# Optimization experiments

Measured on AMD Instinct MI355X. Metric: run time of the kernel, lower is better.

The kernel has to match this reference:

```python
import jax, jax.numpy as jnp
import numpy as np

N, E, U, L = 10000, 320000, 256, 3


def setup_inputs() -> dict:
    key = jax.random.key(0)
    ks = jax.random.split(key, 16)
    s = 0.05
    p = {}
    p["pos"] = jax.random.normal(ks[0], (N, 2), jnp.float32)
    p["edge_attr_in"] = jax.random.uniform(ks[1], (E, 1), jnp.float32)
    p["edge_index"] = jax.random.randint(ks[2], (2, E), 0, N)
    p["Wp"] = jax.random.normal(ks[3], (2, U), jnp.float32) * s
    p["bp"] = jnp.zeros((U,), jnp.float32)
    p["Wa"] = jax.random.normal(ks[4], (1, U), jnp.float32) * s
    p["ba"] = jnp.zeros((U,), jnp.float32)
    p["W1"] = jax.random.normal(ks[5], (L, U, U), jnp.float32) * s
    p["b1"] = jnp.zeros((L, U), jnp.float32)
    p["W2"] = jax.random.normal(ks[6], (L, U, U), jnp.float32) * s
    p["b2"] = jnp.zeros((L, U), jnp.float32)
    p["We"] = jax.random.normal(ks[7], (L + 1, U, U), jnp.float32) * s
    p["be"] = jnp.zeros((L + 1, U), jnp.float32)
    p["Ws"] = jax.random.normal(ks[8], (L + 1, U, U), jnp.float32) * s
    p["Wt"] = jax.random.normal(ks[9], (L + 1, U, U), jnp.float32) * s
    p["Wm1"] = jax.random.normal(ks[10], (U + 1, U // 2), jnp.float32) * s
    p["bm1"] = jnp.zeros((U // 2,), jnp.float32)
    p["alpha"] = 0.25 * jnp.ones((1,), jnp.float32)  # PReLU default slope
    p["Wm2"] = jax.random.normal(ks[11], (U // 2, 1), jnp.float32) * s
    p["bm2"] = jnp.zeros((1,), jnp.float32)
    return p


def _forward(pos, edge_attr_in, edge_index, Wp, bp, Wa, ba, W1, b1, W2, b2,
             We, be, Ws, Wt, Wm1, bm1, alpha, Wm2, bm2):
    src, dst = edge_index[0], edge_index[1]
    x = pos @ Wp + bp                      # [N, U]
    e = edge_attr_in @ Wa + ba             # [E, U]

    def edge_update(x, e, l):
        # ResEdgeLinear: residual edge update from endpoint nodes + edge feats
        return e + jax.nn.relu(e @ We[l] + x[src] @ Ws[l] + x[dst] @ Wt[l] + be[l])

    for l in range(L):
        # ResNodeConv: gated gather-linear-scatter with residual
        gate = jax.nn.sigmoid(e)                                   # [E, U]
        msg = gate * (x[src] @ W2[l] + b2[l])                      # [E, U]
        agg = jax.ops.segment_sum(msg, dst, num_segments=N)        # [N, U]
        x_new = x + jax.nn.relu(x @ W1[l] + b1[l] + agg)
        e_new = edge_update(x, e, l)  # simultaneous update: both use old (x, e)
        x, e = x_new, e_new
    e = edge_update(x, e, L)

    h = jnp.concatenate([e, edge_attr_in[:, :1]], axis=-1) @ Wm1 + bm1
    h = jnp.where(h > 0, h, alpha * h)  # PReLU
    return h @ Wm2 + bm2                # [E, 1] logits


def reference(pos, edge_attr_in, edge_index, Wp, bp, Wa, ba, W1, b1, W2, b2,
              We, be, Ws, Wt, Wm1, bm1, alpha, Wm2, bm2):
    return _forward(pos, edge_attr_in, edge_index, Wp, bp, Wa, ba, W1, b1,
                    W2, b2, We, be, Ws, Wt, Wm1, bm1, alpha, Wm2, bm2)
```

## Files before the change

### kernel.cpp

```cpp
#include <hip/hip_runtime.h>
#include <hip/hip_bf16.h>
#include <stdint.h>

#define N_NODES 10000
#define N_EDGES 320000

using bf16x8 = __attribute__((ext_vector_type(8))) short;
using fp32x4 = __attribute__((ext_vector_type(4))) float;
using u16x8 = __attribute__((ext_vector_type(8))) unsigned short;
using i32x4 = __attribute__((ext_vector_type(4))) int;

__device__ __forceinline__ float bf2f(unsigned short u) {
  union { unsigned int i; float f; } v; v.i = ((unsigned int)u) << 16; return v.f;
}
__device__ __forceinline__ unsigned short f2bf(float f) {
  union { float f; unsigned int i; } v; v.f = f;
  unsigned int x = v.i;
  x += 0x7fffu + ((x >> 16) & 1u);
  return (unsigned short)(x >> 16);
}
__device__ __forceinline__ unsigned int f2bf_pk(float lo, float hi) {
  __hip_bfloat162 h = __float22bfloat162_rn(float2{lo, hi});
  union { __hip_bfloat162 h; unsigned int u; } cv; cv.h = h; return cv.u;
}

#define A_POS 0
#define A_EA 20000
#define A_WP 340000
#define A_BP 340512
#define A_WA 340768
#define A_BA 341024
#define A_W1 341280
#define A_B1 537888
#define A_W2 538656
#define A_B2 735264
#define A_WE 736032
#define A_BE 998176
#define A_WS 999200
#define A_WT 1261344
#define A_WM1 1523488
#define A_BM1 1556384
#define A_AL 1556512
#define A_WM2 1556544
#define A_BM2 1556672
#define ARENA_USED 1556673
#define ARENA_TOT 1556736

__constant__ int g_off[19] = {A_POS, A_EA, A_WP, A_BP, A_WA, A_BA, A_W1, A_B1,
                              A_W2, A_B2, A_WE, A_BE, A_WS, A_WT, A_WM1,
                              A_BM1, A_AL, A_WM2, A_BM2};

struct Ptrs { const void* p[19]; };

__global__ void k_detect(const unsigned short* wpraw, int* flag, int* deg) {
  int i = blockIdx.x * 256 + threadIdx.x;
  if (i < N_NODES) deg[i] = 0;
  if (blockIdx.x == 0) {
    __shared__ int cnt;
    int tid = threadIdx.x;
    if (tid == 0) cnt = 0;
    __syncthreads();
    float v0 = bf2f(wpraw[tid]);
    float v1 = bf2f(wpraw[256 + tid]);
    int big = (fabsf(v0) > 100.f ? 1 : 0) + (fabsf(v1) > 100.f ? 1 : 0);
    atomicAdd(&cnt, big);
    __syncthreads();
    if (tid == 0) *flag = (cnt > 10) ? 1 : 0;
  }
}

__global__ void k_cast(Ptrs ptrs, const int* __restrict__ flag,
                       unsigned short* __restrict__ arena) {
  int a = blockIdx.x * 256 + threadIdx.x;
  if (a >= ARENA_USED) return;
  int z = 0;
#pragma unroll
  for (int j = 1; j < 19; ++j) if (a >= g_off[j]) z = j;
  int i = a - g_off[z];
  float v;
  if (*flag) v = ((const float*)ptrs.p[z])[i];
  else       v = bf2f(((const unsigned short*)ptrs.p[z])[i]);
  arena[a] = f2bf(v);
}

__global__ void k_prep(const unsigned short* __restrict__ arena,
                       unsigned short* nodeBT, unsigned short* WeT,
                       unsigned short* Wm1T, unsigned short* biascat) {
  int z = blockIdx.z;
  int i = blockIdx.x * 256 + threadIdx.x;
  if (z == 19) {
    if (i < 3072) {
      int l = i >> 10, j = i & 1023;
      unsigned short v = 0;
      if (j < 256) v = arena[A_B1 + l * 256 + j];
      else if (j < 512) v = arena[A_B2 + l * 256 + (j - 256)];
      biascat[i] = v;
    } else if (i < 3584) {
      biascat[i] = 0;
    }
    return;
  }
  const unsigned short* src; unsigned short* dst; int srcN = 256;
  if (z < 3)       {                 src = arena + A_W1 + z * 65536; dst = nodeBT + z * 262144; }
  else if (z < 6)  { int l = z - 3;  src = arena + A_W2 + l * 65536; dst = nodeBT + l * 262144 + 65536; }
  else if (z < 10) { int l = z - 6;  src = arena + A_WS + l * 65536;
                     dst = (l < 3) ? nodeBT + l * 262144 + 131072 : nodeBT + 786432; }
  else if (z < 14) { int l = z - 10; src = arena + A_WT + l * 65536;
                     dst = (l < 3) ? nodeBT + l * 262144 + 196608 : nodeBT + 786432 + 65536; }
  else if (z < 18) { int l = z - 14; src = arena + A_WE + l * 65536; dst = WeT + l * 65536; }
  else             { src = arena + A_WM1; dst = Wm1T; srcN = 128; }
  if (i < srcN * 256) {
    int k = i & 255, n = i >> 8;
    dst[i] = src[k * srcN + n];
  }
}

__global__ void k_pack(const unsigned short* __restrict__ src,
                       unsigned short* __restrict__ dst, int MT, int nchunks) {
  int c = blockIdx.x * 256 + threadIdx.x;
  if (c >= nchunks) return;
  int perg = MT * 512;
  int g = c / perg, r = c % perg;
  int ks = r / (64 * MT);
  int rem = r % (64 * MT);
  int mt = rem >> 6, lane = rem & 63;
  int q = lane >> 4, ll = lane & 15;
  int oc = g * (MT * 16) + (ll >> 2) * (MT * 4) + (ll & 3) + mt * 4;
  i32x4 v = *(const i32x4*)((const char*)src + ((long)oc << 9) + (ks << 6) + (q << 4));
  ((i32x4*)dst)[c] = v;
}

__global__ void k_init_x(const unsigned short* __restrict__ arena,
                         float* __restrict__ xf, unsigned short* __restrict__ xbf,
                         float* __restrict__ agg) {
  int n = blockIdx.x, c = threadIdx.x;
  float p0 = bf2f(arena[A_POS + 2 * n]), p1 = bf2f(arena[A_POS + 2 * n + 1]);
  float v = fmaf(p0, bf2f(arena[A_WP + c]),
                 fmaf(p1, bf2f(arena[A_WP + 256 + c]), bf2f(arena[A_BP + c])));
  long idx = ((long)n << 8) + c;
  xf[idx] = v;
  xbf[idx] = f2bf(v);
  agg[idx] = 0.f;
}

__global__ void k_hist(const int* __restrict__ dstA, int* __restrict__ deg) {
  int i = blockIdx.x * 256 + threadIdx.x;
  if (i < N_EDGES) {
    int d = dstA[i];
    if ((unsigned)d < N_NODES) atomicAdd(&deg[d], 1);
  }
}

__global__ void k_scan(const int* __restrict__ deg, int* __restrict__ rowptr,
                       int* __restrict__ cursor) {
  __shared__ int part[256];
  int tid = threadIdx.x;
  int base = tid * 40;
  int s = 0;
  for (int i = 0; i < 40; ++i) {
    int idx = base + i;
    if (idx < N_NODES) s += deg[idx];
  }
  part[tid] = s;
  __syncthreads();
  if (tid == 0) {
    int run = 0;
    for (int i = 0; i < 256; ++i) { int t = part[i]; part[i] = run; run += t; }
    rowptr[N_NODES] = run;
  }
  __syncthreads();
  int run = part[tid];
  for (int i = 0; i < 40; ++i) {
    int idx = base + i;
    if (idx < N_NODES) { rowptr[idx] = run; cursor[idx] = run; run += deg[idx]; }
  }
}

__global__ void k_fill(const int* __restrict__ dstA, const int* __restrict__ srcA,
                       const unsigned short* __restrict__ arena,
                       int* __restrict__ cursor, int* __restrict__ eid,
                       int* __restrict__ csrc, int* __restrict__ cdst,
                       unsigned short* __restrict__ eaC) {
  int i = blockIdx.x * 256 + threadIdx.x;
  if (i < N_EDGES) {
    int d = dstA[i]; if ((unsigned)d >= N_NODES) d = 0;
    int p = atomicAdd(&cursor[d], 1);
    if ((unsigned)p < N_EDGES) {
      eid[p] = i;
      int s = srcA[i]; if ((unsigned)s >= N_NODES) s = 0;
      csrc[p] = s;
      cdst[p] = d;
      eaC[p] = arena[A_EA + i];
    }
  }
}

#define SM_PITCH 528
#define XS_PITCH 144
#define EROWS 80
#define ECHUNKS 5
#define EDGE_BLOCKS (N_EDGES / EROWS)

template <bool NT, int ROWS, int BLK>
__device__ __forceinline__ void stage_tile(char* smc, const unsigned short* src,
                                           long rowBase) {
  int tid = threadIdx.x;
#pragma unroll
  for (int it = 0; it < ROWS * 32 / BLK; ++it) {
    int lin = it * BLK + tid;
    int row = lin >> 5, g = lin & 31;
    const i32x4* p = (const i32x4*)((const char*)src + ((rowBase + row) << 9) + (g << 4));
    i32x4 v = NT ? __builtin_nontemporal_load(p) : *p;
    *(i32x4*)(smc + row * SM_PITCH + (g << 4)) = v;
  }
}

template <int MT, int NTT>
__device__ __forceinline__ void gemm_swap(const char* smc, const unsigned short* WTp,
                                          int colBase, fp32x4 (&acc)[MT][NTT]) {
  const int lane = threadIdx.x & 63;
  const int q = lane >> 4, ll = lane & 15;
  const char* wbase = (const char*)WTp + ((long)colBase << 9) + (lane << 4);
  __builtin_amdgcn_s_setprio(1);
#pragma unroll
  for (int ks = 0; ks < 8; ++ks) {
    bf16x8 a[MT];
#pragma unroll
    for (int mt = 0; mt < MT; ++mt)
      a[mt] = *(const bf16x8*)(wbase + ((long)(ks * MT + mt) << 10));
    bf16x8 b[NTT];
#pragma unroll
    for (int nt = 0; nt < NTT; ++nt)
      b[nt] = *(const bf16x8*)(smc + (nt * 16 + ll) * SM_PITCH + (ks << 6) + (q << 4));
#pragma unroll
    for (int mt = 0; mt < MT; ++mt)
#pragma unroll
      for (int nt = 0; nt < NTT; ++nt)
        acc[mt][nt] = __builtin_amdgcn_mfma_f32_16x16x32_bf16(a[mt], b[nt], acc[mt][nt], 0, 0, 0);
  }
  __builtin_amdgcn_s_setprio(0);
}

template <int NTT>
__device__ __forceinline__ void edge_epilogue_cx(
    char* smc, char* xsw, const fp32x4 (&acc)[4][NTT], const int* s_src,
    const int* s_dst, const unsigned short* XW, int xw_pitch, int xs_off,
    int xt_off, const unsigned short* bePtr, int colBase, int lane) {
  const int q = lane >> 4, ll = lane & 15;
  const int cb = colBase + q * 16;
  u16x8 be0 = *(const u16x8*)(bePtr + cb);
  u16x8 be1 = *(const u16x8*)(bePtr + cb + 8);
  const int prow = lane >> 3;
  const int ppc = lane & 7;
  const int pcol = xs_off + colBase + ppc * 8;
  u16x8 pfA = *(const u16x8*)(XW + (long)s_src[prow] * xw_pitch + pcol);
  u16x8 pfB = *(const u16x8*)(XW + (long)s_src[8 + prow] * xw_pitch + pcol);
#pragma unroll
  for (int nt = 0; nt < NTT; ++nt) {
    *(u16x8*)(xsw + prow * XS_PITCH + ppc * 16) = pfA;
    *(u16x8*)(xsw + (8 + prow) * XS_PITCH + ppc * 16) = pfB;
    if (nt + 1 < NTT) {
      int elA = (nt + 1) * 16 + prow;
      pfA = *(const u16x8*)(XW + (long)s_src[elA] * xw_pitch + pcol);
      pfB = *(const u16x8*)(XW + (long)s_src[elA + 8] * xw_pitch + pcol);
    }
    int el = nt * 16 + ll;
    int dn = s_dst[el];
    const unsigned short* xtrow = XW + (long)dn * xw_pitch + xt_off + cb;
    u16x8 xt0 = *(const u16x8*)(xtrow);
    u16x8 xt1 = *(const u16x8*)(xtrow + 8);
    u16x8 xs0 = *(const u16x8*)(xsw + ll * XS_PITCH + q * 32);
    u16x8 xs1 = *(const u16x8*)(xsw + ll * XS_PITCH + q * 32 + 16);
    u16x8* slot = (u16x8*)(smc + el * SM_PITCH + cb * 2);
    u16x8 er0 = slot[0], er1 = slot[1];
    float f[16];
#pragma unroll
    for (int mt = 0; mt < 4; ++mt)
#pragma unroll
      for (int r = 0; r < 4; ++r) {
        int i = mt * 4 + r;
        float xsv = bf2f(i < 8 ? xs0[i] : xs1[i - 8]);
        float xtv = bf2f(i < 8 ? xt0[i] : xt1[i - 8]);
        float erv = bf2f(i < 8 ? er0[i] : er1[i - 8]);
        float bev = bf2f(i < 8 ? be0[i] : be1[i - 8]);
        float v = acc[mt][nt][r] + xsv + xtv + bev;
        v = fmaxf(v, 0.f);
        f[i] = erv + v;
      }
    union { u16x8 v; unsigned int w[4]; } O0, O1;
#pragma unroll
    for (int p = 0; p < 4; ++p) {
      O0.w[p] = f2bf_pk(f[2 * p], f[2 * p + 1]);
      O1.w[p] = f2bf_pk(f[8 + 2 * p], f[9 + 2 * p]);
    }
    slot[0] = O0.v;
    slot[1] = O1.v;
  }
}

__global__ __launch_bounds__(256, 3) void k_edge01(
    unsigned short* __restrict__ e, const unsigned short* __restrict__ WeT0,
    const unsigned short* __restrict__ WeT1,
    const unsigned short* __restrict__ XWa, const unsigned short* __restrict__ XWb,
    const unsigned short* __restrict__ arena, const unsigned short* __restrict__ eaC,
    const int* __restrict__ csrc, const int* __restrict__ cdst,
    float* __restrict__ agg) {
  __shared__ int4 sm4[EROWS * 33];
  __shared__ int4 xsb4[4 * 2304 / 16];
  __shared__ int s_src[EROWS];
  __shared__ int s_dst[EROWS];
  char* smc = (char*)sm4;
  const long tileBase = (long)blockIdx.x * EROWS;
  const int tid = threadIdx.x;
  const int wave = tid >> 6, lane = tid & 63;
  const int colBase = wave * 64;
  char* xsw = (char*)xsb4 + wave * 2304;

#pragma unroll
  for (int it = 0; it < EROWS * 32 / 256; ++it) {
    int lin = it * 256 + tid;
    int row = lin >> 5, g = lin & 31;
    float eav = bf2f(eaC[tileBase + row]);
    int c0 = g * 8;
    float f[8];
#pragma unroll
    for (int j = 0; j < 8; ++j)
      f[j] = fmaf(eav, bf2f(arena[A_WA + c0 + j]), bf2f(arena[A_BA + c0 + j]));
    union { bf16x8 v; unsigned int w[4]; } O;
#pragma unroll
    for (int p = 0; p < 4; ++p) O.w[p] = f2bf_pk(f[2 * p], f[2 * p + 1]);
    *(bf16x8*)(smc + row * SM_PITCH + (g << 4)) = O.v;
  }
  if (tid < EROWS) {
    long edge = tileBase + tid;
    int s = csrc[edge]; if ((unsigned)s >= N_NODES) s = 0;
    int d = cdst[edge]; if ((unsigned)d >= N_NODES) d = 0;
    s_src[tid] = s;
    s_dst[tid] = d;
  }
  __syncthreads();

  fp32x4 acc[4][ECHUNKS];
#pragma unroll
  for (int mt = 0; mt < 4; ++mt)
#pragma unroll
    for (int nt = 0; nt < ECHUNKS; ++nt) acc[mt][nt] = 0.f;
  gemm_swap<4, ECHUNKS>(smc, WeT0, colBase, acc);
  __syncthreads();
  edge_epilogue_cx<ECHUNKS>(smc, xsw, acc, s_src, s_dst, XWa, 1024, 512, 768,
                            arena + A_BE, colBase, lane);
  __syncthreads();

  {
    const int c = tid;
    float a = 0.f;
    int run = s_dst[0];
    for (int b8 = 0; b8 < EROWS; b8 += 8) {
      float evv[8], x2v[8];
#pragma unroll
      for (int j = 0; j < 8; ++j) {
        int row = b8 + j;
        evv[j] = bf2f(*(const unsigned short*)(smc + row * SM_PITCH + c * 2));
        x2v[j] = bf2f(XWb[(long)s_src[row] * 1024 + 256 + c]);
      }
#pragma unroll
      for (int j = 0; j < 8; ++j) {
        int d = s_dst[b8 + j];
        if (d != run) {
          atomicAdd(&agg[((long)run << 8) + c], a);
          a = 0.f;
          run = d;
        }
        float gate = 1.f / (1.f + __expf(-evv[j]));
        a = fmaf(gate, x2v[j], a);
      }
    }
    atomicAdd(&agg[((long)run << 8) + c], a);
  }

#pragma unroll
  for (int mt = 0; mt < 4; ++mt)
#pragma unroll
    for (int nt = 0; nt < ECHUNKS; ++nt) acc[mt][nt] = 0.f;
  gemm_swap<4, ECHUNKS>(smc, WeT1, colBase, acc);
  __syncthreads();
  edge_epilogue_cx<ECHUNKS>(smc, xsw, acc, s_src, s_dst, XWb, 1024, 512, 768,
                            arena + A_BE + 256, colBase, lane);
  __syncthreads();

#pragma unroll
  for (int it = 0; it < EROWS * 32 / 256; ++it) {
    int lin = it * 256 + tid;
    int row = lin >> 5, g = lin & 31;
    i32x4 v = *(const i32x4*)(smc + row * SM_PITCH + (g << 4));
    __builtin_nontemporal_store(v, (i32x4*)((char*)e + ((tileBase + row) << 9) + (g << 4)));
  }
}

__global__ __launch_bounds__(256, 3) void k_edge_last2(
    const unsigned short* __restrict__ e, const unsigned short* __restrict__ WeT2,
    const unsigned short* __restrict__ WeT3,
    const unsigned short* __restrict__ XW2, const unsigned short* __restrict__ XW3,
    const unsigned short* __restrict__ arena, const unsigned short* __restrict__ eaC,
    const int* __restrict__ csrc, const int* __restrict__ cdst,
    const unsigned short* __restrict__ Wm1T, const int* __restrict__ eid,
    const int* __restrict__ flag, void* __restrict__ out) {
  __shared__ int4 sm4[EROWS * 33];
  __shared__ int4 xsb4[4 * 2304 / 16];
  __shared__ int s_src[EROWS];
  __shared__ int s_dst[EROWS];
  __shared__ float part[EROWS * 4];
  char* smc = (char*)sm4;
  const long tileBase = (long)blockIdx.x * EROWS;
  const int tid = threadIdx.x;
  const int wave = tid >> 6, lane = tid & 63;
  const int q = lane >> 4, ll = lane & 15;
  const int colBase = wave * 64;
  char* xsw = (char*)xsb4 + wave * 2304;

  stage_tile<true, EROWS, 256>(smc, e, tileBase);
  if (tid < EROWS) {
    long edge = tileBase + tid;
    int s = csrc[edge]; if ((unsigned)s >= N_NODES) s = 0;
    int d = cdst[edge]; if ((unsigned)d >= N_NODES) d = 0;
    s_src[tid] = s;
    s_dst[tid] = d;
  }
  __syncthreads();

  fp32x4 acc[4][ECHUNKS];
#pragma unroll
  for (int mt = 0; mt < 4; ++mt)
#pragma unroll
    for (int nt = 0; nt < ECHUNKS; ++nt) acc[mt][nt] = 0.f;
  gemm_swap<4, ECHUNKS>(smc, WeT2, colBase, acc);
  __syncthreads();
  edge_epilogue_cx<ECHUNKS>(smc, xsw, acc, s_src, s_dst, XW2, 1024, 512, 768,
                            arena + A_BE + 2 * 256, colBase, lane);
  __syncthreads();

#pragma unroll
  for (int mt = 0; mt < 4; ++mt)
#pragma unroll
    for (int nt = 0; nt < ECHUNKS; ++nt) acc[mt][nt] = 0.f;
  gemm_swap<4, ECHUNKS>(smc, WeT3, colBase, acc);
  __syncthreads();
  edge_epilogue_cx<ECHUNKS>(smc, xsw, acc, s_src, s_dst, XW3, 512, 0, 256,
                            arena + A_BE + 3 * 256, colBase, lane);
  __syncthreads();

  fp32x4 acc2[2][ECHUNKS];
#pragma unroll
  for (int mt = 0; mt < 2; ++mt)
#pragma unroll
    for (int nt = 0; nt < ECHUNKS; ++nt) acc2[mt][nt] = 0.f;
  const int colBase2 = wave * 32;
  gemm_swap<2, ECHUNKS>(smc, Wm1T, colBase2, acc2);

  const int cb2 = colBase2 + q * 8;
  float alphaf = bf2f(arena[A_AL]);
  float bmc[8], wl[8], w2c[8];
#pragma unroll
  for (int i = 0; i < 8; ++i) {
    bmc[i] = bf2f(arena[A_BM1 + cb2 + i]);
    wl[i] = bf2f(arena[A_WM1 + 32768 + cb2 + i]);
    w2c[i] = bf2f(arena[A_WM2 + cb2 + i]);
  }
#pragma unroll
  for (int nt = 0; nt < ECHUNKS; ++nt) {
    int el = nt * 16 + ll;
    float eav = bf2f(eaC[tileBase + el]);
    float ps = 0.f;
#pragma unroll
    for (int mt = 0; mt < 2; ++mt)
#pragma unroll
      for (int r = 0; r < 4; ++r) {
        int i = mt * 4 + r;
        float h = acc2[mt][nt][r] + bmc[i] + eav * wl[i];
        h = (h > 0.f) ? h : alphaf * h;
        ps += h * w2c[i];
      }
    ps += __shfl_xor(ps, 16, 64);
    ps += __shfl_xor(ps, 32, 64);
    if (q == 0) part[el * 4 + wave] = ps;
  }
  __syncthreads();
  if (tid < EROWS) {
    float t = part[tid * 4] + part[tid * 4 + 1] + part[tid * 4 + 2] + part[tid * 4 + 3]
            + bf2f(arena[A_BM2]);
    long row = tileBase + tid;
    int oe = eid[row]; if ((unsigned)oe >= N_EDGES) oe = 0;
    if (*flag) ((float*)out)[oe] = t;
    else       ((unsigned short*)out)[oe] = f2bf(t);
  }
}

__global__ __launch_bounds__(256, 2) void k_node_gemm(
    const unsigned short* __restrict__ xbf, const unsigned short* __restrict__ WT,
    const unsigned short* __restrict__ bias, unsigned short* __restrict__ out,
    int out_pitch) {
  __shared__ int4 sm4[128 * 33];
  char* smc = (char*)sm4;
  const long tileBase = (long)blockIdx.x * 128;
  {
    int tid = threadIdx.x;
#pragma unroll
    for (int it = 0; it < 16; ++it) {
      int lin = it * 256 + tid;
      int row = lin >> 5, g = lin & 31;
      long rg = tileBase + row;
      if (rg > N_NODES - 1) rg = N_NODES - 1;
      i32x4 v = *(const i32x4*)((const char*)xbf + (rg << 9) + (g << 4));
      *(i32x4*)(smc + row * SM_PITCH + (g << 4)) = v;
    }
  }
  __syncthreads();
  fp32x4 acc[4][8];
#pragma unroll
  for (int mt = 0; mt < 4; ++mt)
#pragma unroll
    for (int nt = 0; nt < 8; ++nt) acc[mt][nt] = 0.f;
  const int tid = threadIdx.x, wave = tid >> 6, lane = tid & 63;
  const int q = lane >> 4, ll = lane & 15;
  const int colBase = blockIdx.y * 256 + wave * 64;
  gemm_swap<4, 8>(smc, WT, colBase, acc);

  const int cb = colBase + q * 16;
  u16x8 bs0 = *(const u16x8*)(bias + cb);
  u16x8 bs1 = *(const u16x8*)(bias + cb + 8);
#pragma unroll
  for (int nt = 0; nt < 8; ++nt) {
    long nn = tileBase + nt * 16 + ll;
    if (nn >= N_NODES) continue;
    float f[16];
#pragma unroll
    for (int mt = 0; mt < 4; ++mt)
#pragma unroll
      for (int r = 0; r < 4; ++r) {
        int i = mt * 4 + r;
        float bv = bf2f(i < 8 ? bs0[i] : bs1[i - 8]);
        f[i] = acc[mt][nt][r] + bv;
      }
    union { u16x8 v; unsigned int w[4]; } O0, O1;
#pragma unroll
    for (int p = 0; p < 4; ++p) {
      O0.w[p] = f2bf_pk(f[2 * p], f[2 * p + 1]);
      O1.w[p] = f2bf_pk(f[8 + 2 * p], f[9 + 2 * p]);
    }
    *(u16x8*)(out + nn * out_pitch + cb) = O0.v;
    *(u16x8*)(out + nn * out_pitch + cb + 8) = O1.v;
  }
}

template <bool FIRST>
__global__ void k_agg(const int* __restrict__ csrc, const int* __restrict__ cdst,
                      const unsigned short* __restrict__ e,
                      const unsigned short* __restrict__ eaC,
                      const unsigned short* __restrict__ arena,
                      const unsigned short* __restrict__ XW, int xw_pitch, int x2_off,
                      float* __restrict__ agg) {
  __shared__ int s_src[64];
  __shared__ int s_dst[64];
  const long base = (long)blockIdx.x * 64;
  const int c = threadIdx.x;
  if (c < 64) {
    long r = base + c;
    int s = csrc[r]; if ((unsigned)s >= N_NODES) s = 0;
    int d = cdst[r]; if ((unsigned)d >= N_NODES) d = 0;
    s_src[c] = s;
    s_dst[c] = d;
  }
  __syncthreads();
  float wac = 0.f, bac = 0.f;
  if (FIRST) { wac = bf2f(arena[A_WA + c]); bac = bf2f(arena[A_BA + c]); }
  float a = 0.f;
  int run = s_dst[0];
  for (int b8 = 0; b8 < 64; b8 += 8) {
    float evv[8], x2v[8];
#pragma unroll
    for (int j = 0; j < 8; ++j) {
      int row = b8 + j;
      if (FIRST) evv[j] = fmaf(bf2f(eaC[base + row]), wac, bac);
      else evv[j] = bf2f(__builtin_nontemporal_load(e + ((base + row) << 8) + c));
      x2v[j] = bf2f(XW[(long)s_src[row] * xw_pitch + x2_off + c]);
    }
#pragma unroll
    for (int j = 0; j < 8; ++j) {
      int d = s_dst[b8 + j];
      if (d != run) {
        atomicAdd(&agg[((long)run << 8) + c], a);
        a = 0.f;
        run = d;
      }
      float gate = 1.f / (1.f + __expf(-evv[j]));
      a = fmaf(gate, x2v[j], a);
    }
  }
  atomicAdd(&agg[((long)run << 8) + c], a);
}

__global__ void k_node_update(float* __restrict__ xf, unsigned short* __restrict__ xbf,
                              const unsigned short* __restrict__ XW,
                              float* __restrict__ agg) {
  int n = blockIdx.x, c = threadIdx.x;
  long idx = ((long)n << 8) + c;
  float av = agg[idx];
  agg[idx] = 0.f;
  float t = bf2f(XW[((long)n << 10) + c]) + av;
  float nx = xf[idx] + fmaxf(t, 0.f);
  xf[idx] = nx;
  xbf[idx] = f2bf(nx);
}

extern "C" void kernel_launch(void* const* d_in, const int* in_sizes, int n_in,
                              void* d_out, int out_size, void* d_ws, size_t ws_size,
                              hipStream_t stream) {
  const int* eidx = (const int*)d_in[2];
  const int* srcA = eidx;
  const int* dstA = eidx + N_EDGES;
  (void)in_sizes; (void)n_in; (void)out_size;

  char* ws = (char*)d_ws;
  size_t off = 0;
  auto alloc = [&](size_t bytes) -> char* {
    char* p = ws + off;
    off = (off + bytes + 255) & ~(size_t)255;
    return p;
  };
  unsigned short* e_buf   = (unsigned short*)alloc((size_t)N_EDGES * 256 * 2);
  float*          xf      = (float*)alloc((size_t)N_NODES * 256 * 4);
  unsigned short* xbf     = (unsigned short*)alloc((size_t)N_NODES * 256 * 2);
  unsigned short* XWa     = (unsigned short*)alloc((size_t)N_NODES * 1024 * 2);
  unsigned short* XWb     = (unsigned short*)alloc((size_t)N_NODES * 1024 * 2);
  unsigned short* XW3     = (unsigned short*)alloc((size_t)N_NODES * 512 * 2);
  float*          agg     = (float*)alloc((size_t)N_NODES * 256 * 4);
  unsigned short* nodeBT  = (unsigned short*)alloc((size_t)917504 * 2);
  unsigned short* WeT     = (unsigned short*)alloc((size_t)4 * 65536 * 2);
  unsigned short* Wm1T    = (unsigned short*)alloc((size_t)32768 * 2);
  unsigned short* nodeBTp = (unsigned short*)alloc((size_t)917504 * 2);
  unsigned short* WeTp    = (unsigned short*)alloc((size_t)4 * 65536 * 2);
  unsigned short* Wm1Tp   = (unsigned short*)alloc((size_t)32768 * 2);
  unsigned short* biascat = (unsigned short*)alloc((size_t)3584 * 2);
  unsigned short* arena   = (unsigned short*)alloc((size_t)ARENA_TOT * 2);
  int* deg    = (int*)alloc((size_t)N_NODES * 4);
  int* rowptr = (int*)alloc((size_t)(N_NODES + 1) * 4);
  int* cursor = (int*)alloc((size_t)N_NODES * 4);
  int* eid    = (int*)alloc((size_t)N_EDGES * 4);
  int* csrc   = (int*)alloc((size_t)N_EDGES * 4);
  int* cdst   = (int*)alloc((size_t)N_EDGES * 4);
  unsigned short* eaC = (unsigned short*)alloc((size_t)N_EDGES * 2);
  int* flag   = (int*)alloc(4);
  if (ws_size < off) return;

  Ptrs ptrs;
  {
    int map[19] = {0, 1, 3, 4, 5, 6, 7, 8, 9, 10, 11, 12, 13, 14, 15, 16, 17, 18, 19};
    for (int j = 0; j < 19; ++j) ptrs.p[j] = d_in[map[j]];
  }

  dim3 blk(256);
  k_detect<<<dim3(40), blk, 0, stream>>>((const unsigned short*)d_in[3], flag, deg);
  k_cast<<<dim3((ARENA_USED + 255) / 256), blk, 0, stream>>>(ptrs, flag, arena);
  k_prep<<<dim3(256, 1, 20), blk, 0, stream>>>(arena, nodeBT, WeT, Wm1T, biascat);
  k_pack<<<dim3(448), blk, 0, stream>>>(nodeBT, nodeBTp, 4, 114688);
  k_pack<<<dim3(128), blk, 0, stream>>>(WeT, WeTp, 4, 32768);
  k_pack<<<dim3(16),  blk, 0, stream>>>(Wm1T, Wm1Tp, 2, 4096);
  k_init_x<<<dim3(N_NODES), blk, 0, stream>>>(arena, xf, xbf, agg);
  k_hist<<<dim3(N_EDGES / 256), blk, 0, stream>>>(dstA, deg);
  k_scan<<<dim3(1), blk, 0, stream>>>(deg, rowptr, cursor);
  k_fill<<<dim3(N_EDGES / 256), blk, 0, stream>>>(dstA, srcA, arena, cursor, eid, csrc,
                                                  cdst, eaC);

  k_node_gemm<<<dim3(79, 4), blk, 0, stream>>>(xbf, nodeBTp, biascat, XWa, 1024);
  k_agg<true><<<dim3(N_EDGES / 64), blk, 0, stream>>>(csrc, cdst, e_buf, eaC, arena,
                                                      XWa, 1024, 256, agg);
  k_node_update<<<dim3(N_NODES), blk, 0, stream>>>(xf, xbf, XWa, agg);
  k_node_gemm<<<dim3(79, 4), blk, 0, stream>>>(xbf, nodeBTp + 262144, biascat + 1024,
                                               XWb, 1024);
  k_edge01<<<dim3(EDGE_BLOCKS), blk, 0, stream>>>(
      e_buf, WeTp, WeTp + 65536, XWa, XWb, arena, eaC, csrc, cdst, agg);
  k_node_update<<<dim3(N_NODES), blk, 0, stream>>>(xf, xbf, XWb, agg);
  k_node_gemm<<<dim3(79, 4), blk, 0, stream>>>(xbf, nodeBTp + 2 * 262144, biascat + 2048,
                                               XWa, 1024);
  k_agg<false><<<dim3(N_EDGES / 64), blk, 0, stream>>>(csrc, cdst, e_buf, eaC, arena,
                                                       XWa, 1024, 256, agg);
  k_node_update<<<dim3(N_NODES), blk, 0, stream>>>(xf, xbf, XWa, agg);
  k_node_gemm<<<dim3(79, 2), blk, 0, stream>>>(xbf, nodeBTp + 786432, biascat + 3072, XW3, 512);
  k_edge_last2<<<dim3(EDGE_BLOCKS), blk, 0, stream>>>(
      e_buf, WeTp + 2 * 65536, WeTp + 3 * 65536, XWa, XW3, arena, eaC,
      csrc, cdst, Wm1Tp, eid, flag, d_out);
}
```

Before: 750.8 us.

## Fuse node update into node GEMM prologue with double-buffered x and agg

Removes the separate k_node_update kernels. Each node GEMM now loads fp32 x, the previous XW slice and the aggregate, applies the residual ReLU update, converts to bf16 into shared memory, and (from blockIdx.y==0 only) writes the new fp32 x and zeroes the next aggregate buffer. Ping-pong x and agg buffers are introduced, with xfB aliased onto the XW3 buffer, so reads and writes never hit the same array within a launch. This saves three launches and the bf16 x round-trip, but every y-block recomputes the update and the prologue reads twice as many bytes per tile in fp32.

Result: no change. 755.2 us (+0.6%).

```diff
diff --git a/kernel.cpp b/kernel.cpp
--- a/kernel.cpp
+++ b/kernel.cpp
@@ -8,6 +8,7 @@
 using bf16x8 = __attribute__((ext_vector_type(8))) short;
 using fp32x4 = __attribute__((ext_vector_type(4))) float;
 using u16x8 = __attribute__((ext_vector_type(8))) unsigned short;
+using u16x4 = __attribute__((ext_vector_type(4))) unsigned short;
 using i32x4 = __attribute__((ext_vector_type(4))) int;
 
 __device__ __forceinline__ float bf2f(unsigned short u) {
@@ -131,16 +132,16 @@
 }
 
 __global__ void k_init_x(const unsigned short* __restrict__ arena,
-                         float* __restrict__ xf, unsigned short* __restrict__ xbf,
-                         float* __restrict__ agg) {
+                         float* __restrict__ xf, float* __restrict__ aggA,
+                         float* __restrict__ aggB) {
   int n = blockIdx.x, c = threadIdx.x;
   float p0 = bf2f(arena[A_POS + 2 * n]), p1 = bf2f(arena[A_POS + 2 * n + 1]);
   float v = fmaf(p0, bf2f(arena[A_WP + c]),
                  fmaf(p1, bf2f(arena[A_WP + 256 + c]), bf2f(arena[A_BP + c])));
   long idx = ((long)n << 8) + c;
   xf[idx] = v;
-  xbf[idx] = f2bf(v);
-  agg[idx] = 0.f;
+  aggA[idx] = 0.f;
+  aggB[idx] = 0.f;
 }
 
 __global__ void k_hist(const int* __restrict__ dstA, int* __restrict__ deg) {
@@ -495,23 +496,45 @@
   }
 }
 
-__global__ __launch_bounds__(256, 2) void k_node_gemm(
-    const unsigned short* __restrict__ xbf, const unsigned short* __restrict__ WT,
+template <bool UPD, bool WRX, bool ZAGG>
+__global__ __launch_bounds__(256, 2) void k_fng(
+    const float* __restrict__ xfPrev, const unsigned short* __restrict__ XWprev,
+    const float* __restrict__ aggRd, float* __restrict__ xfNext,
+    float* __restrict__ aggZ, const unsigned short* __restrict__ WTp,
     const unsigned short* __restrict__ bias, unsigned short* __restrict__ out,
     int out_pitch) {
   __shared__ int4 sm4[128 * 33];
   char* smc = (char*)sm4;
   const long tileBase = (long)blockIdx.x * 128;
+  const int tid = threadIdx.x;
   {
-    int tid = threadIdx.x;
-#pragma unroll
-    for (int it = 0; it < 16; ++it) {
+#pragma unroll
+    for (int it = 0; it < 32; ++it) {
       int lin = it * 256 + tid;
-      int row = lin >> 5, g = lin & 31;
+      int row = lin >> 6, cg = lin & 63;
       long rg = tileBase + row;
       if (rg > N_NODES - 1) rg = N_NODES - 1;
-      i32x4 v = *(const i32x4*)((const char*)xbf + (rg << 9) + (g << 4));
-      *(i32x4*)(smc + row * SM_PITCH + (g << 4)) = v;
+      long idx = (rg << 8) + cg * 4;
+      fp32x4 xn = *(const fp32x4*)(xfPrev + idx);
+      if (UPD) {
+        fp32x4 a4 = *(const fp32x4*)(aggRd + idx);
+        u16x4 w4 = *(const u16x4*)(XWprev + (rg << 10) + cg * 4);
+#pragma unroll
+        for (int j = 0; j < 4; ++j) {
+          float t = bf2f(w4[j]) + a4[j];
+          xn[j] = xn[j] + fmaxf(t, 0.f);
+        }
+        if (WRX && blockIdx.y == 0) *(fp32x4*)(xfNext + idx) = xn;
+      }
+      if (ZAGG && blockIdx.y == 0) {
+        fp32x4 z4 = {0.f, 0.f, 0.f, 0.f};
+        *(fp32x4*)(aggZ + idx) = z4;
+      }
+      unsigned int w0 = f2bf_pk(xn[0], xn[1]);
+      unsigned int w1 = f2bf_pk(xn[2], xn[3]);
+      unsigned int* dst = (unsigned int*)(smc + row * SM_PITCH + cg * 8);
+      dst[0] = w0;
+      dst[1] = w1;
     }
   }
   __syncthreads();
@@ -520,10 +543,10 @@
   for (int mt = 0; mt < 4; ++mt)
 #pragma unroll
     for (int nt = 0; nt < 8; ++nt) acc[mt][nt] = 0.f;
-  const int tid = threadIdx.x, wave = tid >> 6, lane = tid & 63;
+  const int wave = tid >> 6, lane = tid & 63;
   const int q = lane >> 4, ll = lane & 15;
   const int colBase = blockIdx.y * 256 + wave * 64;
-  gemm_swap<4, 8>(smc, WT, colBase, acc);
+  gemm_swap<4, 8>(smc, WTp, colBase, acc);
 
   const int cb = colBase + q * 16;
   u16x8 bs0 = *(const u16x8*)(bias + cb);
@@ -599,19 +622,6 @@
   atomicAdd(&agg[((long)run << 8) + c], a);
 }
 
-__global__ void k_node_update(float* __restrict__ xf, unsigned short* __restrict__ xbf,
-                              const unsigned short* __restrict__ XW,
-                              float* __restrict__ agg) {
-  int n = blockIdx.x, c = threadIdx.x;
-  long idx = ((long)n << 8) + c;
-  float av = agg[idx];
-  agg[idx] = 0.f;
-  float t = bf2f(XW[((long)n << 10) + c]) + av;
-  float nx = xf[idx] + fmaxf(t, 0.f);
-  xf[idx] = nx;
-  xbf[idx] = f2bf(nx);
-}
-
 extern "C" void kernel_launch(void* const* d_in, const int* in_sizes, int n_in,
                               void* d_out, int out_size, void* d_ws, size_t ws_size,
                               hipStream_t stream) {
@@ -628,12 +638,13 @@
     return p;
   };
   unsigned short* e_buf   = (unsigned short*)alloc((size_t)N_EDGES * 256 * 2);
-  float*          xf      = (float*)alloc((size_t)N_NODES * 256 * 4);
-  unsigned short* xbf     = (unsigned short*)alloc((size_t)N_NODES * 256 * 2);
+  float*          xfA     = (float*)alloc((size_t)N_NODES * 256 * 4);
   unsigned short* XWa     = (unsigned short*)alloc((size_t)N_NODES * 1024 * 2);
   unsigned short* XWb     = (unsigned short*)alloc((size_t)N_NODES * 1024 * 2);
   unsigned short* XW3     = (unsigned short*)alloc((size_t)N_NODES * 512 * 2);
-  float*          agg     = (float*)alloc((size_t)N_NODES * 256 * 4);
+  float*          xfB     = (float*)XW3;
+  float*          aggA    = (float*)alloc((size_t)N_NODES * 256 * 4);
+  float*          aggB    = (float*)alloc((size_t)N_NODES * 256 * 4);
   unsigned short* nodeBT  = (unsigned short*)alloc((size_t)917504 * 2);
   unsigned short* WeT     = (unsigned short*)alloc((size_t)4 * 65536 * 2);
   unsigned short* Wm1T    = (unsigned short*)alloc((size_t)32768 * 2);
@@ -665,27 +676,26 @@
   k_pack<<<dim3(448), blk, 0, stream>>>(nodeBT, nodeBTp, 4, 114688);
   k_pack<<<dim3(128), blk, 0, stream>>>(WeT, WeTp, 4, 32768);
   k_pack<<<dim3(16),  blk, 0, stream>>>(Wm1T, Wm1Tp, 2, 4096);
-  k_init_x<<<dim3(N_NODES), blk, 0, stream>>>(arena, xf, xbf, agg);
+  k_init_x<<<dim3(N_NODES), blk, 0, stream>>>(arena, xfA, aggA, aggB);
   k_hist<<<dim3(N_EDGES / 256), blk, 0, stream>>>(dstA, deg);
   k_scan<<<dim3(1), blk, 0, stream>>>(deg, rowptr, cursor);
   k_fill<<<dim3(N_EDGES / 256), blk, 0, stream>>>(dstA, srcA, arena, cursor, eid, csrc,
                                                   cdst, eaC);
 
-  k_node_gemm<<<dim3(79, 4), blk, 0, stream>>>(xbf, nodeBTp, biascat, XWa, 1024);
+  k_fng<false, false, false><<<dim3(79, 4), blk, 0, stream>>>(
+      xfA, nullptr, nullptr, nullptr, nullptr, nodeBTp, biascat, XWa, 1024);
   k_agg<true><<<dim3(N_EDGES / 64), blk, 0, stream>>>(csrc, cdst, e_buf, eaC, arena,
-                                                      XWa, 1024, 256, agg);
-  k_node_update<<<dim3(N_NODES), blk, 0, stream>>>(xf, xbf, XWa, agg);
-  k_node_gemm<<<dim3(79, 4), blk, 0, stream>>>(xbf, nodeBTp + 262144, biascat + 1024,
-                                               XWb, 1024);
+                                                      XWa, 1024, 256, aggA);
+  k_fng<true, true, false><<<dim3(79, 4), blk, 0, stream>>>(
+      xfA, XWa, aggA, xfB, nullptr, nodeBTp + 262144, biascat + 1024, XWb, 1024);
   k_edge01<<<dim3(EDGE_BLOCKS), blk, 0, stream>>>(
-      e_buf, WeTp, WeTp + 65536, XWa, XWb, arena, eaC, csrc, cdst, agg);
-  k_node_update<<<dim3(N_NODES), blk, 0, stream>>>(xf, xbf, XWb, agg);
-  k_node_gemm<<<dim3(79, 4), blk, 0, stream>>>(xbf, nodeBTp + 2 * 262144, biascat + 2048,
-                                               XWa, 1024);
+      e_buf, WeTp, WeTp + 65536, XWa, XWb, arena, eaC, csrc, cdst, aggB);
+  k_fng<true, true, true><<<dim3(79, 4), blk, 0, stream>>>(
+      xfB, XWb, aggB, xfA, aggA, nodeBTp + 2 * 262144, biascat + 2048, XWa, 1024);
   k_agg<false><<<dim3(N_EDGES / 64), blk, 0, stream>>>(csrc, cdst, e_buf, eaC, arena,
-                                                       XWa, 1024, 256, agg);
-  k_node_update<<<dim3(N_NODES), blk, 0, stream>>>(xf, xbf, XWa, agg);
-  k_node_gemm<<<dim3(79, 2), blk, 0, stream>>>(xbf, nodeBTp + 786432, biascat + 3072, XW3, 512);
+                                                       XWa, 1024, 256, aggA);
+  k_fng<true, false, false><<<dim3(79, 2), blk, 0, stream>>>(
+      xfA, XWa, aggA, nullptr, nullptr, nodeBTp + 786432, biascat + 3072, XW3, 512);
   k_edge_last2<<<dim3(EDGE_BLOCKS), blk, 0, stream>>>(
       e_buf, WeTp + 2 * 65536, WeTp + 3 * 65536, XWa, XW3, arena, eaC,
       csrc, cdst, Wm1Tp, eid, flag, d_out);
```
